# Performance work log

Hardware: AMD Instinct MI355X
Metric: run time of the kernel (lower is better)

## Reference

```python
import jax, jax.numpy as jnp
import numpy as np

NUM_HEADS = 12
HEAD_SIZE = 64
HIDDEN = 768


def setup_inputs() -> dict:
    key = jax.random.key(0)
    ks = jax.random.split(key, 5)
    B, S, H = 2, 2048, HIDDEN
    scale_in = 0.02
    return {
        "x": jax.random.normal(ks[0], (B, S, H), dtype=jnp.float32),
        "w_qkv": jax.random.normal(ks[1], (3 * H, H), dtype=jnp.float32) * scale_in,
        "b_qkv": jax.random.normal(ks[2], (3 * H,), dtype=jnp.float32) * scale_in,
        "w_o": jax.random.normal(ks[3], (H, H), dtype=jnp.float32) * scale_in,
        "b_o": jax.random.normal(ks[4], (H,), dtype=jnp.float32) * scale_in,
    }


def reference(x, w_qkv, b_qkv, w_o, b_o):
    B, S, H = x.shape
    nh, hd = NUM_HEADS, HEAD_SIZE
    qkv = x @ w_qkv.T + b_qkv                      # (B, S, 3H)
    Q, K, V = jnp.split(qkv, 3, axis=-1)
    Q = Q.reshape(B, S, nh, hd)
    K = K.reshape(B, S, nh, hd)
    V = V.reshape(B, S, nh, hd)
    # scores: (B, nh, S_q, S_k)
    scores = jnp.einsum('bqhd,bkhd->bhqk', Q, K)
    causal = jnp.triu(jnp.ones((S, S), dtype=bool), k=1)
    scores = jnp.where(causal, -jnp.inf, scores)
    attn = jax.nn.softmax(scores / jnp.sqrt(jnp.float32(hd)), axis=3)
    out = jnp.einsum('bhqk,bkhd->bqhd', attn, V).reshape(B, S, nh * hd)
    return out @ w_o.T + b_o
```

## Files before the change

kernel.cpp:

```cpp
#include <hip/hip_runtime.h>
#include <stdint.h>


#define B_   2
#define S_   2048
#define H_   768
#define NH_  12
#define HD_  64
#define M_   4096
#define K_   768
#define N_QKV 2304
#define QKV_ELEMS (B_*NH_*S_*HD_)
#define SCL_ 0.18033688f

using bf16x8 = __attribute__((ext_vector_type(8))) __bf16;
using f32x4  = __attribute__((ext_vector_type(4))) float;
using f32x16 = __attribute__((ext_vector_type(16))) float;

__device__ inline unsigned short f2bf(float f) {
  unsigned int u = __float_as_uint(f);
  u = (u + 0x7FFFu + ((u >> 16) & 1u)) >> 16;
  return (unsigned short)u;
}
__device__ inline float fexp2(float x) {
  float r; asm("v_exp_f32 %0, %1" : "=v"(r) : "v"(x)); return r;
}
__device__ inline unsigned cvtpk(float lo, float hi) {
  unsigned r; asm("v_cvt_pk_bf16_f32 %0, %1, %2" : "=v"(r) : "v"(lo), "v"(hi)); return r;
}
__device__ inline void gload_lds16(const void* g, void* l) {
  __builtin_amdgcn_global_load_lds((const __attribute__((address_space(1))) void*)g,
                                   (__attribute__((address_space(3))) void*)l, 16, 0, 0);
}
#define VWAIT0() do { asm volatile("s_waitcnt vmcnt(0)" ::: "memory"); \
                      __builtin_amdgcn_sched_barrier(0); } while (0)
#define VWAIT8() do { asm volatile("s_waitcnt vmcnt(8)" ::: "memory"); \
                      __builtin_amdgcn_sched_barrier(0); } while (0)
#define LWAIT0() do { asm volatile("s_waitcnt lgkmcnt(0)" ::: "memory"); \
                      __builtin_amdgcn_sched_barrier(0); } while (0)

__global__ void cast3(const float* __restrict__ s0, unsigned short* __restrict__ d0, int n0f,
                      const float* __restrict__ s1, unsigned short* __restrict__ d1, int n1f,
                      const float* __restrict__ s2, unsigned short* __restrict__ d2, int n2f) {
  int i = blockIdx.x * blockDim.x + threadIdx.x;
  const float* s; unsigned short* d; int j;
  if (i < n0f)                { s = s0; d = d0; j = i; }
  else if (i < n0f + n1f)     { s = s1; d = d1; j = i - n0f; }
  else if (i < n0f + n1f + n2f) { s = s2; d = d2; j = i - n0f - n1f; }
  else return;
  float4 v = reinterpret_cast<const float4*>(s)[j];
  ushort4 o;
  o.x = f2bf(v.x); o.y = f2bf(v.y); o.z = f2bf(v.z); o.w = f2bf(v.w);
  reinterpret_cast<ushort4*>(d)[j] = o;
}

template<int N, int MODE, int GX, int TM>
__global__ __launch_bounds__(256, 3)
void gemm_nt(const unsigned short* __restrict__ A,
             const unsigned short* __restrict__ Bw,
             const float* __restrict__ bias,
             unsigned short* __restrict__ qkv_base,
             float* __restrict__ outp)
{
  __shared__ unsigned short As[TM*64];
  __shared__ unsigned short Bs[128*64];
  const int tid  = threadIdx.x;
  const int lane = tid & 63;
  const int wid  = tid >> 6;
  const int g = lane >> 4, lr = lane & 15;
  const int wm = wid >> 1, wn = wid & 1;
  const int cpx = (GX * (M_/TM)) >> 3;
  const int id  = blockIdx.x;
  const int sw  = (id & 7) * cpx + (id >> 3);
  const int n0 = (sw % GX) * 128;
  const int m0 = (sw / GX) * TM;
  constexpr int NI = TM / 32;

  f32x4 acc[NI][4];
  #pragma unroll
  for (int i = 0; i < NI; ++i)
    #pragma unroll
    for (int j = 0; j < 4; ++j) acc[i][j] = f32x4{0.f, 0.f, 0.f, 0.f};

  for (int k0 = 0; k0 < K_; k0 += 64) {
    #pragma unroll
    for (int it = 0; it < TM/32; ++it) {
      int c = it*256 + wid*64 + lane;
      int row = c >> 3, seg = (c & 7) ^ (row & 7);
      int lb = __builtin_amdgcn_readfirstlane((it*256 + wid*64) * 8);
      gload_lds16(&A[(size_t)(m0 + row) * K_ + k0 + seg*8], &As[lb]);
    }
    #pragma unroll
    for (int it = 0; it < 4; ++it) {
      int c = it*256 + wid*64 + lane;
      int row = c >> 3, seg = (c & 7) ^ (row & 7);
      int lb = __builtin_amdgcn_readfirstlane((it*256 + wid*64) * 8);
      gload_lds16(&Bw[(size_t)(n0 + row) * K_ + k0 + seg*8], &Bs[lb]);
    }
    __syncthreads();
    #pragma unroll
    for (int ks = 0; ks < 2; ++ks) {
      bf16x8 af[NI], bfr[4];
      #pragma unroll
      for (int i = 0; i < NI; ++i) {
        int ra = wm*(TM/2) + i*16 + lr;
        af[i]  = *reinterpret_cast<const bf16x8*>(&As[(ra*8 + ((ks*4+g) ^ (ra&7)))*8]);
      }
      #pragma unroll
      for (int j = 0; j < 4; ++j) {
        int rb = wn*64 + j*16 + lr;
        bfr[j] = *reinterpret_cast<const bf16x8*>(&Bs[(rb*8 + ((ks*4+g) ^ (rb&7)))*8]);
      }
      #pragma unroll
      for (int i = 0; i < NI; ++i)
        #pragma unroll
        for (int j = 0; j < 4; ++j)
          acc[i][j] = __builtin_amdgcn_mfma_f32_16x16x32_bf16(af[i], bfr[j], acc[i][j], 0, 0, 0);
    }
    __syncthreads();
  }

  #pragma unroll
  for (int j = 0; j < 4; ++j) {
    int col = n0 + wn*64 + j*16 + lr;
    float bv = bias[col];
    if constexpr (MODE == 0) {
      int which = col / 768;
      int rem = col - which * 768;
      int h = rem >> 6, d = rem & 63;
      if (which == 0) {
        unsigned short* dst = qkv_base;
        #pragma unroll
        for (int i = 0; i < NI; ++i)
          #pragma unroll
          for (int r = 0; r < 4; ++r) {
            int rowm = m0 + wm*(TM/2) + i*16 + g*4 + r;
            int bb = rowm >> 11, ss = rowm & 2047;
            dst[(((size_t)(bb*NH_ + h))*S_ + ss)*HD_ + d] = f2bf(acc[i][j][r] + bv);
          }
      } else if (which == 1) {
        unsigned short* dst = qkv_base + (size_t)QKV_ELEMS;
        #pragma unroll
        for (int i = 0; i < NI; ++i)
          #pragma unroll
          for (int r = 0; r < 4; ++r) {
            int rowm = m0 + wm*(TM/2) + i*16 + g*4 + r;
            int bb = rowm >> 11, ss = rowm & 2047;
            size_t byteoff = ((size_t)(bb*NH_ + h)*(S_>>5) + (ss>>5))*4096
                           + (size_t)(((d>>3)*32 + (ss&31))*16 + (d&7)*2);
            dst[byteoff >> 1] = f2bf(acc[i][j][r] + bv);
          }
      } else {
        unsigned short* dst = qkv_base + 2*(size_t)QKV_ELEMS;
        #pragma unroll
        for (int i = 0; i < NI; ++i) {
          int rowm = m0 + wm*(TM/2) + i*16 + g*4;
          int bb = rowm >> 11, ss = rowm & 2047;
          unsigned w0 = (unsigned)f2bf(acc[i][j][0] + bv) | ((unsigned)f2bf(acc[i][j][1] + bv) << 16);
          unsigned w1 = (unsigned)f2bf(acc[i][j][2] + bv) | ((unsigned)f2bf(acc[i][j][3] + bv) << 16);
          uint2 u; u.x = w0; u.y = w1;
          size_t byteoff = ((size_t)(bb*NH_ + h)*(S_>>5) + (ss>>5))*4096
                         + (size_t)((((ss&31)>>3)*64 + d)*16 + (ss&7)*2);
          *reinterpret_cast<uint2*>(&dst[byteoff >> 1]) = u;
        }
      }
    } else {
      #pragma unroll
      for (int i = 0; i < NI; ++i)
        #pragma unroll
        for (int r = 0; r < 4; ++r) {
          int rowm = m0 + wm*(TM/2) + i*16 + g*4 + r;
          outp[(size_t)rowm * H_ + col] = acc[i][j][r] + bv;
        }
    }
  }
}

__global__ __launch_bounds__(256, 2)
void attn_fwd(const unsigned short* __restrict__ Qp,
              const unsigned short* __restrict__ Ktp,
              const unsigned short* __restrict__ Vtp,
              unsigned short* __restrict__ attn)
{
  __shared__ __align__(16) char smem[66560];
  float* mlb = (float*)(smem + 65536);

  const int tid = threadIdx.x;
  const int l = tid & 63, w = tid >> 6;
  const int q31 = l & 31, hi = l >> 5;
  const int idx = blockIdx.x;
  const int bh = (idx & 7) + 8 * ((idx >> 3) % 3);
  const int pr = (idx >> 3) / 3;
  const unsigned short* Qh = Qp + (size_t)bh * S_ * HD_;
  const char* Ktb = (const char*)Ktp + (size_t)bh * (S_>>5) * 4096;
  const char* Vtb = (const char*)Vtp + (size_t)bh * (S_>>5) * 4096;
  const int bb = bh / NH_, hh = bh % NH_;

  float* OscW = (float*)(smem + w*16384);

  const int qtH = 63 - pr, qtL = pr;
  const int qrowH = qtH*32 + q31, qrowL = qtL*32 + q31;

  bf16x8 qfH[4], qfL[4];
  #pragma unroll
  for (int ks = 0; ks < 4; ++ks) {
    qfH[ks] = *reinterpret_cast<const bf16x8*>(&Qh[(size_t)qrowH*HD_ + ks*16 + hi*8]);
    qfL[ks] = *reinterpret_cast<const bf16x8*>(&Qh[(size_t)qrowL*HD_ + ks*16 + hi*8]);
  }
  VWAIT0();

  f32x16 oH0, oH1, oL0, oL1;
  #pragma unroll
  for (int r = 0; r < 16; ++r) { oH0[r]=0.f; oH1[r]=0.f; oL0[r]=0.f; oL1[r]=0.f; }
  float lrunH = 0.f, lrunL = 0.f;

  const int p = w;
  const int ntH = ((qtH - p) >> 2) + 1;
  const int ntL = (qtL >= p) ? ((qtL - p) >> 2) + 1 : 0;
  const bool dwH = ((qtH & 3) == p);
  const bool dwL = ((qtL & 3) == p);
  const int ntHm1 = ntH - 1, ntLm1 = ntL - 1;

  const char* kt = Ktb + (size_t)p*4096 + l*16;
  const char* vt = Vtb + (size_t)p*4096 + l*16;

  auto STAGE = [&](int buf) {
    unsigned short* Kb = (unsigned short*)(smem + w*16384 + buf*8192);
    unsigned short* Vb = Kb + 2048;
    gload_lds16(kt,        Kb);
    gload_lds16(kt + 1024, Kb + 512);
    gload_lds16(kt + 2048, Kb + 1024);
    gload_lds16(kt + 3072, Kb + 1536);
    gload_lds16(vt,        Vb);
    gload_lds16(vt + 1024, Vb + 512);
    gload_lds16(vt + 2048, Vb + 1024);
    gload_lds16(vt + 3072, Vb + 1536);
    kt += 16384; vt += 16384;
  };

  STAGE(0);
  if (ntH > 1) STAGE(1);

  for (int i = 0; i < ntH; ++i) {
    if (i == ntHm1) { VWAIT0(); } else { VWAIT8(); }
    unsigned short* Kl = (unsigned short*)(smem + w*16384 + (i & 1)*8192);
    unsigned short* Vl = Kl + 2048;
    bf16x8 k0 = *reinterpret_cast<const bf16x8*>(&Kl[((0+hi)*32 + q31)*8]);
    bf16x8 k1 = *reinterpret_cast<const bf16x8*>(&Kl[((2+hi)*32 + q31)*8]);
    bf16x8 k2 = *reinterpret_cast<const bf16x8*>(&Kl[((4+hi)*32 + q31)*8]);
    bf16x8 k3 = *reinterpret_cast<const bf16x8*>(&Kl[((6+hi)*32 + q31)*8]);
    bf16x8 v0 = *reinterpret_cast<const bf16x8*>(&Vl[((  hi)*64 +      q31)*8]);
    bf16x8 v1 = *reinterpret_cast<const bf16x8*>(&Vl[((2+hi)*64 +      q31)*8]);
    bf16x8 v2 = *reinterpret_cast<const bf16x8*>(&Vl[((  hi)*64 + 32 + q31)*8]);
    bf16x8 v3 = *reinterpret_cast<const bf16x8*>(&Vl[((2+hi)*64 + 32 + q31)*8]);
    LWAIT0();
    if (i + 2 < ntH) STAGE(i & 1);
    asm volatile("" ::: "memory");

    const bool doL = (i < ntL);

    f32x16 sfH;
    #pragma unroll
    for (int r = 0; r < 16; ++r) sfH[r] = 0.f;
    sfH = __builtin_amdgcn_mfma_f32_32x32x16_bf16(k0, qfH[0], sfH, 0, 0, 0);
    sfH = __builtin_amdgcn_mfma_f32_32x32x16_bf16(k1, qfH[1], sfH, 0, 0, 0);
    sfH = __builtin_amdgcn_mfma_f32_32x32x16_bf16(k2, qfH[2], sfH, 0, 0, 0);
    sfH = __builtin_amdgcn_mfma_f32_32x32x16_bf16(k3, qfH[3], sfH, 0, 0, 0);
    f32x16 sfL;
    #pragma unroll
    for (int r = 0; r < 16; ++r) sfL[r] = 0.f;
    if (doL) {
      sfL = __builtin_amdgcn_mfma_f32_32x32x16_bf16(k0, qfL[0], sfL, 0, 0, 0);
      sfL = __builtin_amdgcn_mfma_f32_32x32x16_bf16(k1, qfL[1], sfL, 0, 0, 0);
      sfL = __builtin_amdgcn_mfma_f32_32x32x16_bf16(k2, qfL[2], sfL, 0, 0, 0);
      sfL = __builtin_amdgcn_mfma_f32_32x32x16_bf16(k3, qfL[3], sfL, 0, 0, 0);
    }

    if (dwH && i == ntHm1) {
      const int kv0 = qtH*32;
      #pragma unroll
      for (int r = 0; r < 16; ++r) {
        int kv = kv0 + (r & 3) + 8*(r >> 2) + 4*hi;
        if (kv > qrowH) sfH[r] = -1e38f;
      }
    }
    if (doL && dwL && i == ntLm1) {
      const int kv0 = qtL*32;
      #pragma unroll
      for (int r = 0; r < 16; ++r) {
        int kv = kv0 + (r & 3) + 8*(r >> 2) + 4*hi;
        if (kv > qrowL) sfL[r] = -1e38f;
      }
    }

    #pragma unroll
    for (int r = 0; r < 16; ++r) sfH[r] = fexp2(sfH[r] * SCL_);
    {
      float s0 = (sfH[0]+sfH[1])+(sfH[2]+sfH[3]);
      float s1 = (sfH[4]+sfH[5])+(sfH[6]+sfH[7]);
      float s2 = (sfH[8]+sfH[9])+(sfH[10]+sfH[11]);
      float s3 = (sfH[12]+sfH[13])+(sfH[14]+sfH[15]);
      lrunH += (s0+s1)+(s2+s3);
      unsigned pw0 = cvtpk(sfH[0],sfH[1]),  pw1 = cvtpk(sfH[2],sfH[3]);
      unsigned pw2 = cvtpk(sfH[4],sfH[5]),  pw3 = cvtpk(sfH[6],sfH[7]);
      unsigned pw4 = cvtpk(sfH[8],sfH[9]),  pw5 = cvtpk(sfH[10],sfH[11]);
      unsigned pw6 = cvtpk(sfH[12],sfH[13]), pw7 = cvtpk(sfH[14],sfH[15]);
      asm("v_permlane32_swap_b32 %0, %1" : "+v"(pw0), "+v"(pw2));
      asm("v_permlane32_swap_b32 %0, %1" : "+v"(pw1), "+v"(pw3));
      asm("v_permlane32_swap_b32 %0, %1" : "+v"(pw4), "+v"(pw6));
      asm("v_permlane32_swap_b32 %0, %1" : "+v"(pw5), "+v"(pw7));
      uint4 pf0; pf0.x = pw0; pf0.y = pw1; pf0.z = pw2; pf0.w = pw3;
      uint4 pf1; pf1.x = pw4; pf1.y = pw5; pf1.z = pw6; pf1.w = pw7;
      oH0 = __builtin_amdgcn_mfma_f32_32x32x16_bf16(v0, *reinterpret_cast<bf16x8*>(&pf0), oH0, 0, 0, 0);
      oH0 = __builtin_amdgcn_mfma_f32_32x32x16_bf16(v1, *reinterpret_cast<bf16x8*>(&pf1), oH0, 0, 0, 0);
      oH1 = __builtin_amdgcn_mfma_f32_32x32x16_bf16(v2, *reinterpret_cast<bf16x8*>(&pf0), oH1, 0, 0, 0);
      oH1 = __builtin_amdgcn_mfma_f32_32x32x16_bf16(v3, *reinterpret_cast<bf16x8*>(&pf1), oH1, 0, 0, 0);
    }

    if (doL) {
      #pragma unroll
      for (int r = 0; r < 16; ++r) sfL[r] = fexp2(sfL[r] * SCL_);
      float s0 = (sfL[0]+sfL[1])+(sfL[2]+sfL[3]);
      float s1 = (sfL[4]+sfL[5])+(sfL[6]+sfL[7]);
      float s2 = (sfL[8]+sfL[9])+(sfL[10]+sfL[11]);
      float s3 = (sfL[12]+sfL[13])+(sfL[14]+sfL[15]);
      lrunL += (s0+s1)+(s2+s3);
      unsigned pw0 = cvtpk(sfL[0],sfL[1]),  pw1 = cvtpk(sfL[2],sfL[3]);
      unsigned pw2 = cvtpk(sfL[4],sfL[5]),  pw3 = cvtpk(sfL[6],sfL[7]);
      unsigned pw4 = cvtpk(sfL[8],sfL[9]),  pw5 = cvtpk(sfL[10],sfL[11]);
      unsigned pw6 = cvtpk(sfL[12],sfL[13]), pw7 = cvtpk(sfL[14],sfL[15]);
      asm("v_permlane32_swap_b32 %0, %1" : "+v"(pw0), "+v"(pw2));
      asm("v_permlane32_swap_b32 %0, %1" : "+v"(pw1), "+v"(pw3));
      asm("v_permlane32_swap_b32 %0, %1" : "+v"(pw4), "+v"(pw6));
      asm("v_permlane32_swap_b32 %0, %1" : "+v"(pw5), "+v"(pw7));
      uint4 pf0; pf0.x = pw0; pf0.y = pw1; pf0.z = pw2; pf0.w = pw3;
      uint4 pf1; pf1.x = pw4; pf1.y = pw5; pf1.z = pw6; pf1.w = pw7;
      oL0 = __builtin_amdgcn_mfma_f32_32x32x16_bf16(v0, *reinterpret_cast<bf16x8*>(&pf0), oL0, 0, 0, 0);
      oL0 = __builtin_amdgcn_mfma_f32_32x32x16_bf16(v1, *reinterpret_cast<bf16x8*>(&pf1), oL0, 0, 0, 0);
      oL1 = __builtin_amdgcn_mfma_f32_32x32x16_bf16(v2, *reinterpret_cast<bf16x8*>(&pf0), oL1, 0, 0, 0);
      oL1 = __builtin_amdgcn_mfma_f32_32x32x16_bf16(v3, *reinterpret_cast<bf16x8*>(&pf1), oL1, 0, 0, 0);
    }
  }

  const int q = tid & 31, dseg8 = tid >> 5;

  auto MERGE = [&](const f32x16& a0v, const f32x16& a1v, float lr, int qt) {
    __syncthreads();
    #pragma unroll
    for (int rr = 0; rr < 4; ++rr) {
      f32x4 a;
      #pragma unroll
      for (int e = 0; e < 4; ++e) a[e] = a0v[4*rr + e];
      *reinterpret_cast<f32x4*>(&OscW[q31*36 + 8*rr + 4*hi]) = a;
    }
    mlb[w*64 + hi*32 + q31] = lr;
    __syncthreads();
    float inv;
    {
      float lt = (mlb[q] + mlb[32+q]) + (mlb[64+q] + mlb[96+q])
               + (mlb[128+q] + mlb[160+q]) + (mlb[192+q] + mlb[224+q]);
      inv = 1.f / lt;
    }
    if (dseg8 < 4) {
      const int dd = dseg8*8;
      #define OSC(a, off) (*reinterpret_cast<f32x4*>((float*)(smem + (a)*16384) + (off)))
      f32x4 a0 = OSC(0, q*36 + dd), b0 = OSC(0, q*36 + dd + 4);
      f32x4 a1 = OSC(1, q*36 + dd), b1 = OSC(1, q*36 + dd + 4);
      f32x4 a2 = OSC(2, q*36 + dd), b2 = OSC(2, q*36 + dd + 4);
      f32x4 a3 = OSC(3, q*36 + dd), b3 = OSC(3, q*36 + dd + 4);
      f32x4 ra, rb;
      #pragma unroll
      for (int e = 0; e < 4; ++e) {
        ra[e] = ((a0[e] + a1[e]) + (a2[e] + a3[e])) * inv;
        rb[e] = ((b0[e] + b1[e]) + (b2[e] + b3[e])) * inv;
      }
      uint4 ov;
      ov.x = cvtpk(ra[0], ra[1]); ov.y = cvtpk(ra[2], ra[3]);
      ov.z = cvtpk(rb[0], rb[1]); ov.w = cvtpk(rb[2], rb[3]);
      *reinterpret_cast<uint4*>(&attn[((size_t)(bb*S_ + qt*32 + q))*H_ + hh*HD_ + dd]) = ov;
    }
    __syncthreads();
    #pragma unroll
    for (int rr = 0; rr < 4; ++rr) {
      f32x4 a;
      #pragma unroll
      for (int e = 0; e < 4; ++e) a[e] = a1v[4*rr + e];
      *reinterpret_cast<f32x4*>(&OscW[q31*36 + 8*rr + 4*hi]) = a;
    }
    __syncthreads();
    if (dseg8 >= 4) {
      const int dd = (dseg8 - 4)*8;
      f32x4 a0 = OSC(0, q*36 + dd), b0 = OSC(0, q*36 + dd + 4);
      f32x4 a1 = OSC(1, q*36 + dd), b1 = OSC(1, q*36 + dd + 4);
      f32x4 a2 = OSC(2, q*36 + dd), b2 = OSC(2, q*36 + dd + 4);
      f32x4 a3 = OSC(3, q*36 + dd), b3 = OSC(3, q*36 + dd + 4);
      #undef OSC
      f32x4 ra, rb;
      #pragma unroll
      for (int e = 0; e < 4; ++e) {
        ra[e] = ((a0[e] + a1[e]) + (a2[e] + a3[e])) * inv;
        rb[e] = ((b0[e] + b1[e]) + (b2[e] + b3[e])) * inv;
      }
      uint4 ov;
      ov.x = cvtpk(ra[0], ra[1]); ov.y = cvtpk(ra[2], ra[3]);
      ov.z = cvtpk(rb[0], rb[1]); ov.w = cvtpk(rb[2], rb[3]);
      *reinterpret_cast<uint4*>(&attn[((size_t)(bb*S_ + qt*32 + q))*H_ + hh*HD_ + 32 + dd]) = ov;
    }
    __syncthreads();
  };

  MERGE(oH0, oH1, lrunH, qtH);
  MERGE(oL0, oL1, lrunL, qtL);
}

extern "C" void kernel_launch(void* const* d_in, const int* in_sizes, int n_in,
                              void* d_out, int out_size, void* d_ws, size_t ws_size,
                              hipStream_t stream)
{
  const float* x      = (const float*)d_in[0];
  const float* w_qkv  = (const float*)d_in[1];
  const float* b_qkv  = (const float*)d_in[2];
  const float* w_o    = (const float*)d_in[3];
  const float* b_o    = (const float*)d_in[4];
  float* out = (float*)d_out;

  unsigned short* xb    = (unsigned short*)d_ws;
  unsigned short* wqkvb = xb    + (size_t)M_ * K_;
  unsigned short* wob   = wqkvb + (size_t)N_QKV * K_;
  unsigned short* Qw    = wob   + (size_t)H_ * H_;
  unsigned short* Ktw   = Qw + (size_t)QKV_ELEMS;
  unsigned short* Vtw   = Ktw + (size_t)QKV_ELEMS;
  unsigned short* attn  = Vtw + (size_t)QKV_ELEMS;

  cast3<<<5376, 256, 0, stream>>>(x, xb, 786432,
                                  w_qkv, wqkvb, 442368,
                                  w_o, wob, 147456);
  gemm_nt<N_QKV, 0, 18, 128><<<576, 256, 0, stream>>>(xb, wqkvb, b_qkv, Qw, nullptr);
  attn_fwd<<<dim3(768), 256, 0, stream>>>(Qw, Ktw, Vtw, attn);
  gemm_nt<H_, 1, 6, 64><<<384, 256, 0, stream>>>(attn, wob, b_o, nullptr, out);
}
```

Measured before the change: 71.06 us.

## Fuse fp32 x cast into QKV GEMM and single-buffer attention K/V tiles

Removes the separate bf16 cast of x by having the QKV GEMM load fp32 rows directly, convert with v_cvt_pk_bf16_f32 and write swizzled into LDS. Attention K/V staging drops from double to single buffering, halving shared memory per block to allow more resident blocks. Risks: fp32 A loads are twice the bytes and re-read across column tiles, lose async global-to-LDS loads, and single buffering exposes more load latency per tile.

```diff
diff --git a/kernel.cpp b/kernel.cpp
--- a/kernel.cpp
+++ b/kernel.cpp
@@ -34,19 +34,15 @@
 }
 #define VWAIT0() do { asm volatile("s_waitcnt vmcnt(0)" ::: "memory"); \
                       __builtin_amdgcn_sched_barrier(0); } while (0)
-#define VWAIT8() do { asm volatile("s_waitcnt vmcnt(8)" ::: "memory"); \
-                      __builtin_amdgcn_sched_barrier(0); } while (0)
 #define LWAIT0() do { asm volatile("s_waitcnt lgkmcnt(0)" ::: "memory"); \
                       __builtin_amdgcn_sched_barrier(0); } while (0)
 
-__global__ void cast3(const float* __restrict__ s0, unsigned short* __restrict__ d0, int n0f,
-                      const float* __restrict__ s1, unsigned short* __restrict__ d1, int n1f,
+__global__ void cast2(const float* __restrict__ s1, unsigned short* __restrict__ d1, int n1f,
                       const float* __restrict__ s2, unsigned short* __restrict__ d2, int n2f) {
   int i = blockIdx.x * blockDim.x + threadIdx.x;
   const float* s; unsigned short* d; int j;
-  if (i < n0f)                { s = s0; d = d0; j = i; }
-  else if (i < n0f + n1f)     { s = s1; d = d1; j = i - n0f; }
-  else if (i < n0f + n1f + n2f) { s = s2; d = d2; j = i - n0f - n1f; }
+  if (i < n1f)            { s = s1; d = d1; j = i; }
+  else if (i < n1f + n2f) { s = s2; d = d2; j = i - n1f; }
   else return;
   float4 v = reinterpret_cast<const float4*>(s)[j];
   ushort4 o;
@@ -54,9 +50,9 @@
   reinterpret_cast<ushort4*>(d)[j] = o;
 }
 
-template<int N, int MODE, int GX, int TM>
+template<int N, int MODE, int GX, int TM, bool AF32>
 __global__ __launch_bounds__(256, 3)
-void gemm_nt(const unsigned short* __restrict__ A,
+void gemm_nt(const void* __restrict__ Ain,
              const unsigned short* __restrict__ Bw,
              const float* __restrict__ bias,
              unsigned short* __restrict__ qkv_base,
@@ -83,12 +79,29 @@
     for (int j = 0; j < 4; ++j) acc[i][j] = f32x4{0.f, 0.f, 0.f, 0.f};
 
   for (int k0 = 0; k0 < K_; k0 += 64) {
-    #pragma unroll
-    for (int it = 0; it < TM/32; ++it) {
-      int c = it*256 + wid*64 + lane;
-      int row = c >> 3, seg = (c & 7) ^ (row & 7);
-      int lb = __builtin_amdgcn_readfirstlane((it*256 + wid*64) * 8);
-      gload_lds16(&A[(size_t)(m0 + row) * K_ + k0 + seg*8], &As[lb]);
+    if constexpr (AF32) {
+      const float* Af = (const float*)Ain;
+      #pragma unroll
+      for (int it = 0; it < TM/32; ++it) {
+        int c = it*256 + tid;
+        int row = c >> 3, seg = (c & 7) ^ (row & 7);
+        const float* src = &Af[(size_t)(m0 + row) * K_ + k0 + seg*8];
+        float4 a = *reinterpret_cast<const float4*>(src);
+        float4 b = *reinterpret_cast<const float4*>(src + 4);
+        uint4 pk;
+        pk.x = cvtpk(a.x, a.y); pk.y = cvtpk(a.z, a.w);
+        pk.z = cvtpk(b.x, b.y); pk.w = cvtpk(b.z, b.w);
+        *reinterpret_cast<uint4*>(&As[c*8]) = pk;
+      }
+    } else {
+      const unsigned short* Ab = (const unsigned short*)Ain;
+      #pragma unroll
+      for (int it = 0; it < TM/32; ++it) {
+        int c = it*256 + wid*64 + lane;
+        int row = c >> 3, seg = (c & 7) ^ (row & 7);
+        int lb = __builtin_amdgcn_readfirstlane((it*256 + wid*64) * 8);
+        gload_lds16(&Ab[(size_t)(m0 + row) * K_ + k0 + seg*8], &As[lb]);
+      }
     }
     #pragma unroll
     for (int it = 0; it < 4; ++it) {
@@ -182,8 +195,8 @@
               const unsigned short* __restrict__ Vtp,
               unsigned short* __restrict__ attn)
 {
-  __shared__ __align__(16) char smem[66560];
-  float* mlb = (float*)(smem + 65536);
+  __shared__ __align__(16) char smem[34816];
+  float* mlb = (float*)(smem + 32768);
 
   const int tid = threadIdx.x;
   const int l = tid & 63, w = tid >> 6;
@@ -196,7 +209,9 @@
   const char* Vtb = (const char*)Vtp + (size_t)bh * (S_>>5) * 4096;
   const int bb = bh / NH_, hh = bh % NH_;
 
-  float* OscW = (float*)(smem + w*16384);
+  unsigned short* Kl = (unsigned short*)(smem + w*8192);
+  unsigned short* Vl = Kl + 2048;
+  float* OscW = (float*)(smem + w*8192);
 
   const int qtH = 63 - pr, qtL = pr;
   const int qrowH = qtH*32 + q31, qrowL = qtL*32 + q31;
@@ -207,7 +222,6 @@
     qfH[ks] = *reinterpret_cast<const bf16x8*>(&Qh[(size_t)qrowH*HD_ + ks*16 + hi*8]);
     qfL[ks] = *reinterpret_cast<const bf16x8*>(&Qh[(size_t)qrowL*HD_ + ks*16 + hi*8]);
   }
-  VWAIT0();
 
   f32x16 oH0, oH1, oL0, oL1;
   #pragma unroll
@@ -224,27 +238,22 @@
   const char* kt = Ktb + (size_t)p*4096 + l*16;
   const char* vt = Vtb + (size_t)p*4096 + l*16;
 
-  auto STAGE = [&](int buf) {
-    unsigned short* Kb = (unsigned short*)(smem + w*16384 + buf*8192);
-    unsigned short* Vb = Kb + 2048;
-    gload_lds16(kt,        Kb);
-    gload_lds16(kt + 1024, Kb + 512);
-    gload_lds16(kt + 2048, Kb + 1024);
-    gload_lds16(kt + 3072, Kb + 1536);
-    gload_lds16(vt,        Vb);
-    gload_lds16(vt + 1024, Vb + 512);
-    gload_lds16(vt + 2048, Vb + 1024);
-    gload_lds16(vt + 3072, Vb + 1536);
+  auto STAGE = [&]() {
+    gload_lds16(kt,        Kl);
+    gload_lds16(kt + 1024, Kl + 512);
+    gload_lds16(kt + 2048, Kl + 1024);
+    gload_lds16(kt + 3072, Kl + 1536);
+    gload_lds16(vt,        Vl);
+    gload_lds16(vt + 1024, Vl + 512);
+    gload_lds16(vt + 2048, Vl + 1024);
+    gload_lds16(vt + 3072, Vl + 1536);
     kt += 16384; vt += 16384;
   };
 
-  STAGE(0);
-  if (ntH > 1) STAGE(1);
+  STAGE();
 
   for (int i = 0; i < ntH; ++i) {
-    if (i == ntHm1) { VWAIT0(); } else { VWAIT8(); }
-    unsigned short* Kl = (unsigned short*)(smem + w*16384 + (i & 1)*8192);
-    unsigned short* Vl = Kl + 2048;
+    VWAIT0();
     bf16x8 k0 = *reinterpret_cast<const bf16x8*>(&Kl[((0+hi)*32 + q31)*8]);
     bf16x8 k1 = *reinterpret_cast<const bf16x8*>(&Kl[((2+hi)*32 + q31)*8]);
     bf16x8 k2 = *reinterpret_cast<const bf16x8*>(&Kl[((4+hi)*32 + q31)*8]);
@@ -254,7 +263,7 @@
     bf16x8 v2 = *reinterpret_cast<const bf16x8*>(&Vl[((  hi)*64 + 32 + q31)*8]);
     bf16x8 v3 = *reinterpret_cast<const bf16x8*>(&Vl[((2+hi)*64 + 32 + q31)*8]);
     LWAIT0();
-    if (i + 2 < ntH) STAGE(i & 1);
+    if (i + 1 < ntH) STAGE();
     asm volatile("" ::: "memory");
 
     const bool doL = (i < ntL);
@@ -363,7 +372,7 @@
     }
     if (dseg8 < 4) {
       const int dd = dseg8*8;
-      #define OSC(a, off) (*reinterpret_cast<f32x4*>((float*)(smem + (a)*16384) + (off)))
+      #define OSC(a, off) (*reinterpret_cast<f32x4*>((float*)(smem + (a)*8192) + (off)))
       f32x4 a0 = OSC(0, q*36 + dd), b0 = OSC(0, q*36 + dd + 4);
       f32x4 a1 = OSC(1, q*36 + dd), b1 = OSC(1, q*36 + dd + 4);
       f32x4 a2 = OSC(2, q*36 + dd), b2 = OSC(2, q*36 + dd + 4);
@@ -424,18 +433,16 @@
   const float* b_o    = (const float*)d_in[4];
   float* out = (float*)d_out;
 
-  unsigned short* xb    = (unsigned short*)d_ws;
-  unsigned short* wqkvb = xb    + (size_t)M_ * K_;
+  unsigned short* wqkvb = (unsigned short*)d_ws;
   unsigned short* wob   = wqkvb + (size_t)N_QKV * K_;
   unsigned short* Qw    = wob   + (size_t)H_ * H_;
   unsigned short* Ktw   = Qw + (size_t)QKV_ELEMS;
   unsigned short* Vtw   = Ktw + (size_t)QKV_ELEMS;
   unsigned short* attn  = Vtw + (size_t)QKV_ELEMS;
 
-  cast3<<<5376, 256, 0, stream>>>(x, xb, 786432,
-                                  w_qkv, wqkvb, 442368,
+  cast2<<<2304, 256, 0, stream>>>(w_qkv, wqkvb, 442368,
                                   w_o, wob, 147456);
-  gemm_nt<N_QKV, 0, 18, 128><<<576, 256, 0, stream>>>(xb, wqkvb, b_qkv, Qw, nullptr);
+  gemm_nt<N_QKV, 0, 18, 128, true><<<576, 256, 0, stream>>>(x, wqkvb, b_qkv, Qw, nullptr);
   attn_fwd<<<dim3(768), 256, 0, stream>>>(Qw, Ktw, Vtw, attn);
-  gemm_nt<H_, 1, 6, 64><<<384, 256, 0, stream>>>(attn, wob, b_o, nullptr, out);
-}
+  gemm_nt<H_, 1, 6, 64, false><<<384, 256, 0, stream>>>(attn, wob, b_o, nullptr, out);
+}
```

Measured after the change: 76.43 us. +7.5%, slower.

## Drop double-buffered K/V staging to halve attention LDS footprint

Applied to the files above, without the earlier changes.

The attention kernel moves from a two-deep K/V prefetch ring in LDS to a single buffer per wave, cutting shared memory from about 65KB to about 34KB. Each iteration now waits for all outstanding loads and then issues the next tile's load after the fragments have been read into registers. The smaller footprint could let more blocks fit per CU, but the load for the next tile now has only one iteration's compute to hide behind. The per-wave output scratch region is shrunk to match.

```diff
diff --git a/kernel.cpp b/kernel.cpp
--- a/kernel.cpp
+++ b/kernel.cpp
@@ -33,8 +33,6 @@
                                    (__attribute__((address_space(3))) void*)l, 16, 0, 0);
 }
 #define VWAIT0() do { asm volatile("s_waitcnt vmcnt(0)" ::: "memory"); \
-                      __builtin_amdgcn_sched_barrier(0); } while (0)
-#define VWAIT8() do { asm volatile("s_waitcnt vmcnt(8)" ::: "memory"); \
                       __builtin_amdgcn_sched_barrier(0); } while (0)
 #define LWAIT0() do { asm volatile("s_waitcnt lgkmcnt(0)" ::: "memory"); \
                       __builtin_amdgcn_sched_barrier(0); } while (0)
@@ -182,8 +180,8 @@
               const unsigned short* __restrict__ Vtp,
               unsigned short* __restrict__ attn)
 {
-  __shared__ __align__(16) char smem[66560];
-  float* mlb = (float*)(smem + 65536);
+  __shared__ __align__(16) char smem[34816];
+  float* mlb = (float*)(smem + 32768);
 
   const int tid = threadIdx.x;
   const int l = tid & 63, w = tid >> 6;
@@ -196,7 +194,9 @@
   const char* Vtb = (const char*)Vtp + (size_t)bh * (S_>>5) * 4096;
   const int bb = bh / NH_, hh = bh % NH_;
 
-  float* OscW = (float*)(smem + w*16384);
+  unsigned short* Kl = (unsigned short*)(smem + w*8192);
+  unsigned short* Vl = Kl + 2048;
+  float* OscW = (float*)(smem + w*8192);
 
   const int qtH = 63 - pr, qtL = pr;
   const int qrowH = qtH*32 + q31, qrowL = qtL*32 + q31;
@@ -207,7 +207,6 @@
     qfH[ks] = *reinterpret_cast<const bf16x8*>(&Qh[(size_t)qrowH*HD_ + ks*16 + hi*8]);
     qfL[ks] = *reinterpret_cast<const bf16x8*>(&Qh[(size_t)qrowL*HD_ + ks*16 + hi*8]);
   }
-  VWAIT0();
 
   f32x16 oH0, oH1, oL0, oL1;
   #pragma unroll
@@ -224,27 +223,22 @@
   const char* kt = Ktb + (size_t)p*4096 + l*16;
   const char* vt = Vtb + (size_t)p*4096 + l*16;
 
-  auto STAGE = [&](int buf) {
-    unsigned short* Kb = (unsigned short*)(smem + w*16384 + buf*8192);
-    unsigned short* Vb = Kb + 2048;
-    gload_lds16(kt,        Kb);
-    gload_lds16(kt + 1024, Kb + 512);
-    gload_lds16(kt + 2048, Kb + 1024);
-    gload_lds16(kt + 3072, Kb + 1536);
-    gload_lds16(vt,        Vb);
-    gload_lds16(vt + 1024, Vb + 512);
-    gload_lds16(vt + 2048, Vb + 1024);
-    gload_lds16(vt + 3072, Vb + 1536);
+  auto STAGE = [&]() {
+    gload_lds16(kt,        Kl);
+    gload_lds16(kt + 1024, Kl + 512);
+    gload_lds16(kt + 2048, Kl + 1024);
+    gload_lds16(kt + 3072, Kl + 1536);
+    gload_lds16(vt,        Vl);
+    gload_lds16(vt + 1024, Vl + 512);
+    gload_lds16(vt + 2048, Vl + 1024);
+    gload_lds16(vt + 3072, Vl + 1536);
     kt += 16384; vt += 16384;
   };
 
-  STAGE(0);
-  if (ntH > 1) STAGE(1);
+  STAGE();
 
   for (int i = 0; i < ntH; ++i) {
-    if (i == ntHm1) { VWAIT0(); } else { VWAIT8(); }
-    unsigned short* Kl = (unsigned short*)(smem + w*16384 + (i & 1)*8192);
-    unsigned short* Vl = Kl + 2048;
+    VWAIT0();
     bf16x8 k0 = *reinterpret_cast<const bf16x8*>(&Kl[((0+hi)*32 + q31)*8]);
     bf16x8 k1 = *reinterpret_cast<const bf16x8*>(&Kl[((2+hi)*32 + q31)*8]);
     bf16x8 k2 = *reinterpret_cast<const bf16x8*>(&Kl[((4+hi)*32 + q31)*8]);
@@ -254,7 +248,7 @@
     bf16x8 v2 = *reinterpret_cast<const bf16x8*>(&Vl[((  hi)*64 + 32 + q31)*8]);
     bf16x8 v3 = *reinterpret_cast<const bf16x8*>(&Vl[((2+hi)*64 + 32 + q31)*8]);
     LWAIT0();
-    if (i + 2 < ntH) STAGE(i & 1);
+    if (i + 1 < ntH) STAGE();
     asm volatile("" ::: "memory");
 
     const bool doL = (i < ntL);
@@ -363,7 +357,7 @@
     }
     if (dseg8 < 4) {
       const int dd = dseg8*8;
-      #define OSC(a, off) (*reinterpret_cast<f32x4*>((float*)(smem + (a)*16384) + (off)))
+      #define OSC(a, off) (*reinterpret_cast<f32x4*>((float*)(smem + (a)*8192) + (off)))
       f32x4 a0 = OSC(0, q*36 + dd), b0 = OSC(0, q*36 + dd + 4);
       f32x4 a1 = OSC(1, q*36 + dd), b1 = OSC(1, q*36 + dd + 4);
       f32x4 a2 = OSC(2, q*36 + dd), b2 = OSC(2, q*36 + dd + 4);
```

After: 69.88 us, median of 3. No clear change (-1.7%).
